# Kernel tuning notes

Hardware: AMD Instinct MI355X
Metric: run time of the kernel (lower is better)

The kernel has to match this reference:

```python
import jax, jax.numpy as jnp
import numpy as np

B, S, E, H = 2, 2048, 1024, 16
D = E // H


def setup_inputs() -> dict:
    key = jax.random.key(0)
    ks = jax.random.split(key, 11)
    inp = {
        "query": jax.random.normal(ks[0], (B, S, E), jnp.float32),
        "key": jax.random.normal(ks[1], (B, S, E), jnp.float32),
        "value": jax.random.normal(ks[2], (B, S, E), jnp.float32),
        "mask": jnp.tril(jnp.ones((S, S), bool))[None, None],  # causal [1,1,S,S]
    }
    sc = 1.0 / np.sqrt(E)
    inp["Wq"] = jax.random.uniform(ks[3], (E, E), jnp.float32, -sc, sc)
    inp["bq"] = jax.random.uniform(ks[4], (E,), jnp.float32, -sc, sc)
    inp["Wk"] = jax.random.uniform(ks[5], (E, E), jnp.float32, -sc, sc)
    inp["bk"] = jax.random.uniform(ks[6], (E,), jnp.float32, -sc, sc)
    inp["Wv"] = jax.random.uniform(ks[7], (E, E), jnp.float32, -sc, sc)
    inp["bv"] = jax.random.uniform(ks[8], (E,), jnp.float32, -sc, sc)
    inp["Wo"] = jax.random.uniform(ks[9], (E, E), jnp.float32, -sc, sc)
    inp["bo"] = jax.random.uniform(ks[10], (E,), jnp.float32, -sc, sc)
    return inp


def reference(query, key, value, mask, Wq, bq, Wk, bk, Wv, bv, Wo, bo):
    def proj(x, W, b):  # torch Linear: x @ W.T + b, then split heads -> [B,H,S,D]
        y = jnp.einsum("bse,fe->bsf", x, W) + b
        return y.reshape(B, S, H, D).transpose(0, 2, 1, 3)

    q = proj(query, Wq, bq)
    k = proj(key, Wk, bk)
    v = proj(value, Wv, bv)
    scores = jnp.einsum("bhqd,bhkd->bhqk", q, k) / jnp.sqrt(jnp.float32(D))
    scores = jnp.where(mask, scores, jnp.float32(-1e9))
    attn = jax.nn.softmax(scores, axis=-1)  # [B,H,S,S]
    out = jnp.einsum("bhqk,bhkd->bhqd", attn, v)
    out = out.transpose(0, 2, 1, 3).reshape(B, S, E)
    out = jnp.einsum("bse,fe->bsf", out, Wo) + bo
    return out, attn
```

## Files before the change

kernel.cpp:

```cpp
#include <hip/hip_runtime.h>
#include <hip/hip_bf16.h>

#define BB 2
#define SS 2048
#define EE 1024
#define HH 16
#define DD 64

typedef __attribute__((ext_vector_type(8))) short short8;
typedef __attribute__((ext_vector_type(4))) float f32x4;

__device__ __forceinline__ unsigned short f2bf(float f) {
    unsigned int u = __builtin_bit_cast(unsigned int, f);
    u += 0x7fffu + ((u >> 16) & 1u);
    return (unsigned short)(u >> 16);
}

template<bool A_BF16, int OUT_MODE>
__global__ __launch_bounds__(256)
void proj_gemm(const void* __restrict__ Aptr, const float* __restrict__ W,
               const float* __restrict__ bias, void* __restrict__ Cptr)
{
    constexpr int K = EE;
    __shared__ unsigned short As[64][40];
    __shared__ unsigned short Bs[64][40];
    const int t = threadIdx.x;
    const int lane = t & 63;
    const int w = t >> 6;
    const int wm = w >> 1, wn = w & 1;
    const int m0 = blockIdx.y * 64;
    const int n0 = blockIdx.x * 64;

    const int srow = t >> 2;
    const int skc  = (t & 3) * 8;

    f32x4 acc[2][2] = {};

    for (int k0 = 0; k0 < K; k0 += 32) {
        if (A_BF16) {
            const unsigned short* Ab = (const unsigned short*)Aptr;
            short8 pk = *reinterpret_cast<const short8*>(Ab + (size_t)(m0 + srow) * K + k0 + skc);
            *reinterpret_cast<short8*>(&As[srow][skc]) = pk;
        } else {
            const float* Af = (const float*)Aptr;
            f32x4 v0 = *reinterpret_cast<const f32x4*>(Af + (size_t)(m0 + srow) * K + k0 + skc);
            f32x4 v1 = *reinterpret_cast<const f32x4*>(Af + (size_t)(m0 + srow) * K + k0 + skc + 4);
            short8 pk;
            #pragma unroll
            for (int i = 0; i < 4; i++) { pk[i] = (short)f2bf(v0[i]); pk[i + 4] = (short)f2bf(v1[i]); }
            *reinterpret_cast<short8*>(&As[srow][skc]) = pk;
        }
        {
            f32x4 v0 = *reinterpret_cast<const f32x4*>(W + (size_t)(n0 + srow) * K + k0 + skc);
            f32x4 v1 = *reinterpret_cast<const f32x4*>(W + (size_t)(n0 + srow) * K + k0 + skc + 4);
            short8 pk;
            #pragma unroll
            for (int i = 0; i < 4; i++) { pk[i] = (short)f2bf(v0[i]); pk[i + 4] = (short)f2bf(v1[i]); }
            *reinterpret_cast<short8*>(&Bs[srow][skc]) = pk;
        }
        __syncthreads();

        const int fr = lane & 15;
        const int fk = (lane >> 4) * 8;
        short8 a[2], b[2];
        a[0] = *reinterpret_cast<const short8*>(&As[wm * 32 + fr][fk]);
        a[1] = *reinterpret_cast<const short8*>(&As[wm * 32 + 16 + fr][fk]);
        b[0] = *reinterpret_cast<const short8*>(&Bs[wn * 32 + fr][fk]);
        b[1] = *reinterpret_cast<const short8*>(&Bs[wn * 32 + 16 + fr][fk]);
        #pragma unroll
        for (int i = 0; i < 2; i++)
            #pragma unroll
            for (int j = 0; j < 2; j++)
                acc[i][j] = __builtin_amdgcn_mfma_f32_16x16x32_bf16(a[i], b[j], acc[i][j], 0, 0, 0);
        __syncthreads();
    }

    #pragma unroll
    for (int j = 0; j < 2; j++) {
        const int col = n0 + wn * 32 + j * 16 + (lane & 15);
        const float bsv = bias[col];
        #pragma unroll
        for (int i = 0; i < 2; i++) {
            #pragma unroll
            for (int r = 0; r < 4; r++) {
                const int row = m0 + wm * 32 + i * 16 + (lane >> 4) * 4 + r;
                float y = acc[i][j][r] + bsv;
                if (OUT_MODE == 1) {
                    ((float*)Cptr)[(size_t)row * EE + col] = y;
                } else {
                    const int b_ = row >> 11, s_ = row & (SS - 1);
                    const int h_ = col >> 6,  d_ = col & 63;
                    if (OUT_MODE == 0)
                        ((unsigned short*)Cptr)[((size_t)(b_ * HH + h_) * SS + s_) * DD + d_] = f2bf(y);
                    else
                        ((unsigned short*)Cptr)[((size_t)(b_ * HH + h_) * DD + d_) * SS + s_] = f2bf(y);
                }
            }
        }
    }
}

__global__ __launch_bounds__(256)
void attn_kernel(const unsigned short* __restrict__ Q, const unsigned short* __restrict__ Kb,
                 const unsigned short* __restrict__ Vt, float* __restrict__ attn,
                 unsigned short* __restrict__ attnout)
{
    const int t = threadIdx.x;
    const int lane = t & 63;
    const int w = t >> 6;
    const int bh = blockIdx.y;
    const int b_ = bh >> 4, h_ = bh & 15;
    const int q0 = blockIdx.x * 64 + w * 16;

    __shared__ unsigned short Pst[4][16][40];

    const int fr  = lane & 15;
    const int fkg = lane >> 4;
    const size_t qkbase = (size_t)bh * SS * DD;

    short8 aq0 = *reinterpret_cast<const short8*>(Q + qkbase + (size_t)(q0 + fr) * DD + fkg * 8);
    short8 aq1 = *reinterpret_cast<const short8*>(Q + qkbase + (size_t)(q0 + fr) * DD + 32 + fkg * 8);

    const int nkt = q0 / 16 + 1;

    float lsum[4] = {0.f, 0.f, 0.f, 0.f};
    for (int kt = 0; kt < nkt; kt++) {
        short8 bk0 = *reinterpret_cast<const short8*>(Kb + qkbase + (size_t)(kt * 16 + fr) * DD + fkg * 8);
        short8 bk1 = *reinterpret_cast<const short8*>(Kb + qkbase + (size_t)(kt * 16 + fr) * DD + 32 + fkg * 8);
        f32x4 sc = {};
        sc = __builtin_amdgcn_mfma_f32_16x16x32_bf16(aq0, bk0, sc, 0, 0, 0);
        sc = __builtin_amdgcn_mfma_f32_16x16x32_bf16(aq1, bk1, sc, 0, 0, 0);
        const int col = kt * 16 + fr;
        #pragma unroll
        for (int r = 0; r < 4; r++) {
            const int row = q0 + fkg * 4 + r;
            lsum[r] += (col <= row) ? __expf(sc[r] * 0.125f) : 0.0f;
        }
    }
    #pragma unroll
    for (int r = 0; r < 4; r++) {
        #pragma unroll
        for (int off = 1; off < 16; off <<= 1)
            lsum[r] += __shfl_xor(lsum[r], off, 64);
    }
    float inv_l[4];
    #pragma unroll
    for (int r = 0; r < 4; r++) inv_l[r] = 1.0f / lsum[r];

    f32x4 accv[4] = {};
    const size_t attnbase = (size_t)bh * SS * SS;
    const int nktp = (nkt + 1) >> 1;
    for (int ktp = 0; ktp < nktp; ktp++) {
        #pragma unroll
        for (int half = 0; half < 2; half++) {
            const int kt = ktp * 2 + half;
            if (kt < nkt) {
                short8 bk0 = *reinterpret_cast<const short8*>(Kb + qkbase + (size_t)(kt * 16 + fr) * DD + fkg * 8);
                short8 bk1 = *reinterpret_cast<const short8*>(Kb + qkbase + (size_t)(kt * 16 + fr) * DD + 32 + fkg * 8);
                f32x4 sc = {};
                sc = __builtin_amdgcn_mfma_f32_16x16x32_bf16(aq0, bk0, sc, 0, 0, 0);
                sc = __builtin_amdgcn_mfma_f32_16x16x32_bf16(aq1, bk1, sc, 0, 0, 0);
                const int col = kt * 16 + fr;
                #pragma unroll
                for (int r = 0; r < 4; r++) {
                    const int row = q0 + fkg * 4 + r;
                    const float p = (col <= row) ? __expf(sc[r] * 0.125f) * inv_l[r] : 0.0f;
                    attn[attnbase + (size_t)row * SS + col] = p;
                    Pst[w][fkg * 4 + r][half * 16 + fr] = f2bf(p);
                }
            } else {
                #pragma unroll
                for (int r = 0; r < 4; r++)
                    Pst[w][fkg * 4 + r][half * 16 + fr] = 0;
            }
        }
        short8 pa = *reinterpret_cast<const short8*>(&Pst[w][fr][fkg * 8]);
        #pragma unroll
        for (int n = 0; n < 4; n++) {
            short8 bvv = *reinterpret_cast<const short8*>(
                Vt + (size_t)bh * DD * SS + (size_t)(n * 16 + fr) * SS + ktp * 32 + fkg * 8);
            accv[n] = __builtin_amdgcn_mfma_f32_16x16x32_bf16(pa, bvv, accv[n], 0, 0, 0);
        }
    }

    #pragma unroll 1
    for (int r16 = 0; r16 < 16; r16++) {
        float* dst = attn + attnbase + (size_t)(q0 + r16) * SS;
        for (int c = nkt * 16 + lane * 4; c < SS; c += 256) {
            f32x4 z = {};
            *reinterpret_cast<f32x4*>(dst + c) = z;
        }
    }

    #pragma unroll
    for (int n = 0; n < 4; n++) {
        #pragma unroll
        for (int r = 0; r < 4; r++) {
            const int row = q0 + fkg * 4 + r;
            const int e = h_ * 64 + n * 16 + fr;
            attnout[(size_t)(b_ * SS + row) * EE + e] = f2bf(accv[n][r]);
        }
    }
}

extern "C" void kernel_launch(void* const* d_in, const int* in_sizes, int n_in,
                              void* d_out, int out_size, void* d_ws, size_t ws_size,
                              hipStream_t stream) {
    const float* query = (const float*)d_in[0];
    const float* key   = (const float*)d_in[1];
    const float* value = (const float*)d_in[2];
    const float* Wq = (const float*)d_in[4];
    const float* bq = (const float*)d_in[5];
    const float* Wk = (const float*)d_in[6];
    const float* bk = (const float*)d_in[7];
    const float* Wv = (const float*)d_in[8];
    const float* bvp = (const float*)d_in[9];
    const float* Wo = (const float*)d_in[10];
    const float* bo = (const float*)d_in[11];

    float* out  = (float*)d_out;
    float* attn = out + (size_t)BB * SS * EE;

    unsigned short* qb  = (unsigned short*)d_ws;
    unsigned short* kb  = qb  + (size_t)BB * HH * SS * DD;
    unsigned short* vtb = kb  + (size_t)BB * HH * SS * DD;
    unsigned short* aob = vtb + (size_t)BB * HH * SS * DD;

    dim3 gg(EE / 64, (BB * SS) / 64);
    proj_gemm<false, 0><<<gg, 256, 0, stream>>>(query, Wq, bq, qb);
    proj_gemm<false, 0><<<gg, 256, 0, stream>>>(key,   Wk, bk, kb);
    proj_gemm<false, 2><<<gg, 256, 0, stream>>>(value, Wv, bvp, vtb);
    attn_kernel<<<dim3(SS / 64, BB * HH), 256, 0, stream>>>(qb, kb, vtb, attn, aob);
    proj_gemm<true, 1><<<gg, 256, 0, stream>>>(aob, Wo, bo, out);
}
```

Before: 1.047 ms.

## Pre-convert inputs to bf16, use 128x128 LDS-DMA GEMM, transpose attention MFMA

Adds standalone fp32-to-bf16 conversion kernels for the inputs and weights, staging the results in the attention output buffer before it is written. Replaces the 64x64 projection GEMM with a 128x128 tile GEMM that loads bf16 tiles directly into LDS via global_load_lds, giving more reuse per tile. The attention kernel swaps the MFMA operand order so each lane holds one query row, which allows vectorized attn stores and a cheaper row-sum reduction. It also launches query blocks in reverse order so the longest causal blocks start first. These changes target redundant per-tile conversion, low arithmetic intensity, scattered stores and causal load imbalance, at the cost of extra conversion passes and scratch traffic.

```diff
diff --git a/kernel.cpp b/kernel.cpp
--- a/kernel.cpp
+++ b/kernel.cpp
@@ -8,6 +8,7 @@
 #define DD 64
 
 typedef __attribute__((ext_vector_type(8))) short short8;
+typedef __attribute__((ext_vector_type(4))) short s16x4;
 typedef __attribute__((ext_vector_type(4))) float f32x4;
 
 __device__ __forceinline__ unsigned short f2bf(float f) {
@@ -16,74 +17,101 @@
     return (unsigned short)(u >> 16);
 }
 
-template<bool A_BF16, int OUT_MODE>
+__device__ __forceinline__ void gload_lds16(const void* g, void* l) {
+    __builtin_amdgcn_global_load_lds(
+        (const __attribute__((address_space(1))) void*)g,
+        (__attribute__((address_space(3))) void*)l, 16, 0, 0);
+}
+
 __global__ __launch_bounds__(256)
-void proj_gemm(const void* __restrict__ Aptr, const float* __restrict__ W,
-               const float* __restrict__ bias, void* __restrict__ Cptr)
+void cvt_bf16(const float* __restrict__ src, unsigned short* __restrict__ dst, int n8) {
+    int i = blockIdx.x * blockDim.x + threadIdx.x;
+    if (i < n8) {
+        f32x4 v0 = *reinterpret_cast<const f32x4*>(src + (size_t)i * 8);
+        f32x4 v1 = *reinterpret_cast<const f32x4*>(src + (size_t)i * 8 + 4);
+        short8 pk;
+        #pragma unroll
+        for (int j = 0; j < 4; j++) { pk[j] = (short)f2bf(v0[j]); pk[j + 4] = (short)f2bf(v1[j]); }
+        *reinterpret_cast<short8*>(dst + (size_t)i * 8) = pk;
+    }
+}
+
+template<bool B_F32, int OUT_MODE>
+__global__ __launch_bounds__(256)
+void gemm128(const unsigned short* __restrict__ A, const void* __restrict__ Wp,
+             const float* __restrict__ bias, void* __restrict__ Cptr)
 {
     constexpr int K = EE;
-    __shared__ unsigned short As[64][40];
-    __shared__ unsigned short Bs[64][40];
+    __shared__ unsigned short As[128 * 32];
+    __shared__ unsigned short Bs[128 * 32];
     const int t = threadIdx.x;
     const int lane = t & 63;
     const int w = t >> 6;
     const int wm = w >> 1, wn = w & 1;
-    const int m0 = blockIdx.y * 64;
-    const int n0 = blockIdx.x * 64;
-
-    const int srow = t >> 2;
-    const int skc  = (t & 3) * 8;
-
-    f32x4 acc[2][2] = {};
+    const int m0 = blockIdx.y * 128;
+    const int n0 = blockIdx.x * 128;
+    const int fr = lane & 15;
+    const int fkg = lane >> 4;
+    const int grow = lane >> 2;
+    const int gcol = (lane & 3) * 8;
+
+    f32x4 acc[4][4] = {};
 
     for (int k0 = 0; k0 < K; k0 += 32) {
-        if (A_BF16) {
-            const unsigned short* Ab = (const unsigned short*)Aptr;
-            short8 pk = *reinterpret_cast<const short8*>(Ab + (size_t)(m0 + srow) * K + k0 + skc);
-            *reinterpret_cast<short8*>(&As[srow][skc]) = pk;
+        #pragma unroll
+        for (int c = 0; c < 2; c++) {
+            const int chunk = w * 2 + c;
+            gload_lds16(A + (size_t)(m0 + chunk * 16 + grow) * K + k0 + gcol,
+                        &As[chunk * 512]);
+        }
+        if (!B_F32) {
+            const unsigned short* Wb = (const unsigned short*)Wp;
+            #pragma unroll
+            for (int c = 0; c < 2; c++) {
+                const int chunk = w * 2 + c;
+                gload_lds16(Wb + (size_t)(n0 + chunk * 16 + grow) * K + k0 + gcol,
+                            &Bs[chunk * 512]);
+            }
         } else {
-            const float* Af = (const float*)Aptr;
-            f32x4 v0 = *reinterpret_cast<const f32x4*>(Af + (size_t)(m0 + srow) * K + k0 + skc);
-            f32x4 v1 = *reinterpret_cast<const f32x4*>(Af + (size_t)(m0 + srow) * K + k0 + skc + 4);
-            short8 pk;
-            #pragma unroll
-            for (int i = 0; i < 4; i++) { pk[i] = (short)f2bf(v0[i]); pk[i + 4] = (short)f2bf(v1[i]); }
-            *reinterpret_cast<short8*>(&As[srow][skc]) = pk;
-        }
-        {
-            f32x4 v0 = *reinterpret_cast<const f32x4*>(W + (size_t)(n0 + srow) * K + k0 + skc);
-            f32x4 v1 = *reinterpret_cast<const f32x4*>(W + (size_t)(n0 + srow) * K + k0 + skc + 4);
-            short8 pk;
-            #pragma unroll
-            for (int i = 0; i < 4; i++) { pk[i] = (short)f2bf(v0[i]); pk[i + 4] = (short)f2bf(v1[i]); }
-            *reinterpret_cast<short8*>(&Bs[srow][skc]) = pk;
+            const float* Wf = (const float*)Wp;
+            const int row = t >> 1;
+            const int c0 = (t & 1) * 16;
+            #pragma unroll
+            for (int u = 0; u < 2; u++) {
+                f32x4 v0 = *reinterpret_cast<const f32x4*>(Wf + (size_t)(n0 + row) * K + k0 + c0 + u * 8);
+                f32x4 v1 = *reinterpret_cast<const f32x4*>(Wf + (size_t)(n0 + row) * K + k0 + c0 + u * 8 + 4);
+                short8 pk;
+                #pragma unroll
+                for (int j = 0; j < 4; j++) { pk[j] = (short)f2bf(v0[j]); pk[j + 4] = (short)f2bf(v1[j]); }
+                *reinterpret_cast<short8*>(&Bs[row * 32 + c0 + u * 8]) = pk;
+            }
         }
         __syncthreads();
 
-        const int fr = lane & 15;
-        const int fk = (lane >> 4) * 8;
-        short8 a[2], b[2];
-        a[0] = *reinterpret_cast<const short8*>(&As[wm * 32 + fr][fk]);
-        a[1] = *reinterpret_cast<const short8*>(&As[wm * 32 + 16 + fr][fk]);
-        b[0] = *reinterpret_cast<const short8*>(&Bs[wn * 32 + fr][fk]);
-        b[1] = *reinterpret_cast<const short8*>(&Bs[wn * 32 + 16 + fr][fk]);
-        #pragma unroll
-        for (int i = 0; i < 2; i++)
-            #pragma unroll
-            for (int j = 0; j < 2; j++)
+        short8 a[4], b[4];
+        #pragma unroll
+        for (int i = 0; i < 4; i++)
+            a[i] = *reinterpret_cast<const short8*>(&As[(wm * 64 + i * 16 + fr) * 32 + fkg * 8]);
+        #pragma unroll
+        for (int j = 0; j < 4; j++)
+            b[j] = *reinterpret_cast<const short8*>(&Bs[(wn * 64 + j * 16 + fr) * 32 + fkg * 8]);
+        #pragma unroll
+        for (int i = 0; i < 4; i++)
+            #pragma unroll
+            for (int j = 0; j < 4; j++)
                 acc[i][j] = __builtin_amdgcn_mfma_f32_16x16x32_bf16(a[i], b[j], acc[i][j], 0, 0, 0);
         __syncthreads();
     }
 
     #pragma unroll
-    for (int j = 0; j < 2; j++) {
-        const int col = n0 + wn * 32 + j * 16 + (lane & 15);
+    for (int j = 0; j < 4; j++) {
+        const int col = n0 + wn * 64 + j * 16 + fr;
         const float bsv = bias[col];
         #pragma unroll
-        for (int i = 0; i < 2; i++) {
+        for (int i = 0; i < 4; i++) {
             #pragma unroll
             for (int r = 0; r < 4; r++) {
-                const int row = m0 + wm * 32 + i * 16 + (lane >> 4) * 4 + r;
+                const int row = m0 + wm * 64 + i * 16 + fkg * 4 + r;
                 float y = acc[i][j][r] + bsv;
                 if (OUT_MODE == 1) {
                     ((float*)Cptr)[(size_t)row * EE + col] = y;
@@ -110,76 +138,74 @@
     const int w = t >> 6;
     const int bh = blockIdx.y;
     const int b_ = bh >> 4, h_ = bh & 15;
-    const int q0 = blockIdx.x * 64 + w * 16;
+    const int qblk = gridDim.x - 1 - blockIdx.x;
+    const int q0 = qblk * 64 + w * 16;
 
     __shared__ unsigned short Pst[4][16][40];
 
-    const int fr  = lane & 15;
+    const int fr = lane & 15;
     const int fkg = lane >> 4;
     const size_t qkbase = (size_t)bh * SS * DD;
 
-    short8 aq0 = *reinterpret_cast<const short8*>(Q + qkbase + (size_t)(q0 + fr) * DD + fkg * 8);
-    short8 aq1 = *reinterpret_cast<const short8*>(Q + qkbase + (size_t)(q0 + fr) * DD + 32 + fkg * 8);
+    short8 bq0 = *reinterpret_cast<const short8*>(Q + qkbase + (size_t)(q0 + fr) * DD + fkg * 8);
+    short8 bq1 = *reinterpret_cast<const short8*>(Q + qkbase + (size_t)(q0 + fr) * DD + 32 + fkg * 8);
 
     const int nkt = q0 / 16 + 1;
-
-    float lsum[4] = {0.f, 0.f, 0.f, 0.f};
+    const int q = q0 + fr;
+
+    float lsum = 0.f;
+    #pragma unroll 2
     for (int kt = 0; kt < nkt; kt++) {
-        short8 bk0 = *reinterpret_cast<const short8*>(Kb + qkbase + (size_t)(kt * 16 + fr) * DD + fkg * 8);
-        short8 bk1 = *reinterpret_cast<const short8*>(Kb + qkbase + (size_t)(kt * 16 + fr) * DD + 32 + fkg * 8);
+        short8 ak0 = *reinterpret_cast<const short8*>(Kb + qkbase + (size_t)(kt * 16 + fr) * DD + fkg * 8);
+        short8 ak1 = *reinterpret_cast<const short8*>(Kb + qkbase + (size_t)(kt * 16 + fr) * DD + 32 + fkg * 8);
         f32x4 sc = {};
-        sc = __builtin_amdgcn_mfma_f32_16x16x32_bf16(aq0, bk0, sc, 0, 0, 0);
-        sc = __builtin_amdgcn_mfma_f32_16x16x32_bf16(aq1, bk1, sc, 0, 0, 0);
-        const int col = kt * 16 + fr;
+        sc = __builtin_amdgcn_mfma_f32_16x16x32_bf16(ak0, bq0, sc, 0, 0, 0);
+        sc = __builtin_amdgcn_mfma_f32_16x16x32_bf16(ak1, bq1, sc, 0, 0, 0);
         #pragma unroll
         for (int r = 0; r < 4; r++) {
-            const int row = q0 + fkg * 4 + r;
-            lsum[r] += (col <= row) ? __expf(sc[r] * 0.125f) : 0.0f;
-        }
-    }
-    #pragma unroll
-    for (int r = 0; r < 4; r++) {
-        #pragma unroll
-        for (int off = 1; off < 16; off <<= 1)
-            lsum[r] += __shfl_xor(lsum[r], off, 64);
-    }
-    float inv_l[4];
-    #pragma unroll
-    for (int r = 0; r < 4; r++) inv_l[r] = 1.0f / lsum[r];
+            const int k = kt * 16 + fkg * 4 + r;
+            lsum += (k <= q) ? __expf(sc[r] * 0.125f) : 0.0f;
+        }
+    }
+    lsum += __shfl_xor(lsum, 16, 64);
+    lsum += __shfl_xor(lsum, 32, 64);
+    const float inv_l = 1.0f / lsum;
 
     f32x4 accv[4] = {};
     const size_t attnbase = (size_t)bh * SS * SS;
+    const size_t vbase = (size_t)bh * DD * SS;
     const int nktp = (nkt + 1) >> 1;
     for (int ktp = 0; ktp < nktp; ktp++) {
         #pragma unroll
         for (int half = 0; half < 2; half++) {
             const int kt = ktp * 2 + half;
             if (kt < nkt) {
-                short8 bk0 = *reinterpret_cast<const short8*>(Kb + qkbase + (size_t)(kt * 16 + fr) * DD + fkg * 8);
-                short8 bk1 = *reinterpret_cast<const short8*>(Kb + qkbase + (size_t)(kt * 16 + fr) * DD + 32 + fkg * 8);
+                short8 ak0 = *reinterpret_cast<const short8*>(Kb + qkbase + (size_t)(kt * 16 + fr) * DD + fkg * 8);
+                short8 ak1 = *reinterpret_cast<const short8*>(Kb + qkbase + (size_t)(kt * 16 + fr) * DD + 32 + fkg * 8);
                 f32x4 sc = {};
-                sc = __builtin_amdgcn_mfma_f32_16x16x32_bf16(aq0, bk0, sc, 0, 0, 0);
-                sc = __builtin_amdgcn_mfma_f32_16x16x32_bf16(aq1, bk1, sc, 0, 0, 0);
-                const int col = kt * 16 + fr;
+                sc = __builtin_amdgcn_mfma_f32_16x16x32_bf16(ak0, bq0, sc, 0, 0, 0);
+                sc = __builtin_amdgcn_mfma_f32_16x16x32_bf16(ak1, bq1, sc, 0, 0, 0);
+                f32x4 p;
+                s16x4 pb;
                 #pragma unroll
                 for (int r = 0; r < 4; r++) {
-                    const int row = q0 + fkg * 4 + r;
-                    const float p = (col <= row) ? __expf(sc[r] * 0.125f) * inv_l[r] : 0.0f;
-                    attn[attnbase + (size_t)row * SS + col] = p;
-                    Pst[w][fkg * 4 + r][half * 16 + fr] = f2bf(p);
+                    const int k = kt * 16 + fkg * 4 + r;
+                    p[r] = (k <= q) ? __expf(sc[r] * 0.125f) * inv_l : 0.0f;
+                    pb[r] = (short)f2bf(p[r]);
                 }
+                *reinterpret_cast<f32x4*>(attn + attnbase + (size_t)q * SS + kt * 16 + fkg * 4) = p;
+                *reinterpret_cast<s16x4*>(&Pst[w][fr][half * 16 + fkg * 4]) = pb;
             } else {
-                #pragma unroll
-                for (int r = 0; r < 4; r++)
-                    Pst[w][fkg * 4 + r][half * 16 + fr] = 0;
+                s16x4 z = {};
+                *reinterpret_cast<s16x4*>(&Pst[w][fr][half * 16 + fkg * 4]) = z;
             }
         }
         short8 pa = *reinterpret_cast<const short8*>(&Pst[w][fr][fkg * 8]);
         #pragma unroll
         for (int n = 0; n < 4; n++) {
-            short8 bvv = *reinterpret_cast<const short8*>(
-                Vt + (size_t)bh * DD * SS + (size_t)(n * 16 + fr) * SS + ktp * 32 + fkg * 8);
-            accv[n] = __builtin_amdgcn_mfma_f32_16x16x32_bf16(pa, bvv, accv[n], 0, 0, 0);
+            short8 bv = *reinterpret_cast<const short8*>(
+                Vt + vbase + (size_t)(n * 16 + fr) * SS + ktp * 32 + fkg * 8);
+            accv[n] = __builtin_amdgcn_mfma_f32_16x16x32_bf16(pa, bv, accv[n], 0, 0, 0);
         }
     }
 
@@ -221,15 +247,35 @@
     float* out  = (float*)d_out;
     float* attn = out + (size_t)BB * SS * EE;
 
+    const size_t NIN = (size_t)BB * SS * EE;
+    const size_t NW  = (size_t)EE * EE;
+
     unsigned short* qb  = (unsigned short*)d_ws;
-    unsigned short* kb  = qb  + (size_t)BB * HH * SS * DD;
-    unsigned short* vtb = kb  + (size_t)BB * HH * SS * DD;
-    unsigned short* aob = vtb + (size_t)BB * HH * SS * DD;
-
-    dim3 gg(EE / 64, (BB * SS) / 64);
-    proj_gemm<false, 0><<<gg, 256, 0, stream>>>(query, Wq, bq, qb);
-    proj_gemm<false, 0><<<gg, 256, 0, stream>>>(key,   Wk, bk, kb);
-    proj_gemm<false, 2><<<gg, 256, 0, stream>>>(value, Wv, bvp, vtb);
+    unsigned short* kb  = qb  + NIN;
+    unsigned short* vtb = kb  + NIN;
+    unsigned short* aob = vtb + NIN;
+
+    unsigned short* qf  = (unsigned short*)attn;
+    unsigned short* kf  = qf + NIN;
+    unsigned short* vf  = kf + NIN;
+    unsigned short* wqb = vf + NIN;
+    unsigned short* wkb = wqb + NW;
+    unsigned short* wvb = wkb + NW;
+
+    const int n8in = (int)(NIN / 8), n8w = (int)(NW / 8);
+    cvt_bf16<<<n8in / 256, 256, 0, stream>>>(query, qf, n8in);
+    cvt_bf16<<<n8in / 256, 256, 0, stream>>>(key,   kf, n8in);
+    cvt_bf16<<<n8in / 256, 256, 0, stream>>>(value, vf, n8in);
+    cvt_bf16<<<n8w / 256, 256, 0, stream>>>(Wq, wqb, n8w);
+    cvt_bf16<<<n8w / 256, 256, 0, stream>>>(Wk, wkb, n8w);
+    cvt_bf16<<<n8w / 256, 256, 0, stream>>>(Wv, wvb, n8w);
+
+    dim3 gg(EE / 128, (BB * SS) / 128);
+    gemm128<false, 0><<<gg, 256, 0, stream>>>(qf, wqb, bq, qb);
+    gemm128<false, 0><<<gg, 256, 0, stream>>>(kf, wkb, bk, kb);
+    gemm128<false, 2><<<gg, 256, 0, stream>>>(vf, wvb, bvp, vtb);
+
     attn_kernel<<<dim3(SS / 64, BB * HH), 256, 0, stream>>>(qb, kb, vtb, attn, aob);
-    proj_gemm<true, 1><<<gg, 256, 0, stream>>>(aob, Wo, bo, out);
-}
+
+    gemm128<true, 1><<<gg, 256, 0, stream>>>(aob, Wo, bo, out);
+}
```

New measurement: 1.027 ms. Within noise of the previous version (-1.9%).
